# Optimization experiments

Measured on AMD Instinct MI355X. Metric: run time of the kernel, lower is better.

## Reference

```python
import jax, jax.numpy as jnp
import numpy as np

IN, OUT, RANK, ALPHA, GS = 4096, 4096, 16, 32, 64
SCALING = ALPHA / RANK  # alpha / rank = 2.0


def setup_inputs() -> dict:
    key = jax.random.key(0)
    k1, k2, k3, k4, k5 = jax.random.split(key, 5)
    x = jax.random.normal(k1, (4, 2048, IN), dtype=jnp.float32)
    # signed int4 codes in [-8, 7]
    q_w = jax.random.randint(k2, (OUT, IN), -8, 8, dtype=jnp.int32)
    # per-group absmax scales (positive, small)
    scales = jax.random.uniform(k3, (OUT, IN // GS), dtype=jnp.float32) * 0.02 + 1e-3
    lora_A = jax.random.normal(k4, (RANK, IN), dtype=jnp.float32) * 0.02
    lora_B = jax.random.normal(k5, (OUT, RANK), dtype=jnp.float32) * 0.02
    return {"x": x, "q_w": q_w, "scales": scales, "lora_A": lora_A, "lora_B": lora_B}


def reference(x, q_w, scales, lora_A, lora_B):
    # Dequantize 4-bit base weight: blockwise symmetric, group_size=GS along in_features.
    # W[o, g*GS + j] = q[o, g*GS + j] * scales[o, g]
    W = (q_w.astype(jnp.float32).reshape(OUT, IN // GS, GS)
         * scales[:, :, None]).reshape(OUT, IN)
    # Frozen base layer: y = x @ W^T (Linear4bit, no bias)
    base_output = jnp.einsum('bsi,oi->bso', x, W)
    # LoRA branch (dropout p=0 -> identity): B(A(x)) * (alpha/rank)
    lora_output = jnp.einsum('bsr,or->bso', jnp.einsum('bsi,ri->bsr', x, lora_A), lora_B) * SCALING
    return base_output + lora_output
```

## Files before the change

kernel.cpp:

```cpp
#include <hip/hip_runtime.h>
#include <hip/hip_bf16.h>


typedef unsigned short u16;
typedef __attribute__((ext_vector_type(8))) short bf16x8;
typedef __attribute__((ext_vector_type(4))) float f32x4;
typedef __attribute__((ext_vector_type(4))) int i32x4;

#define M_DIM 8192
#define N_DIM 4096
#define K_DIM 4096
#define BK 64
#define KT_MAIN 64
#define NT 65

__device__ static inline u16 f2bf(float f) {
    union { float f; unsigned u; } v; v.f = f;
    unsigned r = v.u + 0x7fffu + ((v.u >> 16) & 1u);
    return (u16)(r >> 16);
}

__device__ static inline void gload16(const void* g, void* s) {
    __builtin_amdgcn_global_load_lds(
        (const __attribute__((address_space(1))) void*)g,
        (__attribute__((address_space(3))) void*)s, 16, 0, 0);
}

__global__ __launch_bounds__(256) void prep_kernel(
        const int* __restrict__ q, const float* __restrict__ scales,
        const float* __restrict__ lora_B, const float* __restrict__ x,
        const float* __restrict__ lora_A,
        u16* __restrict__ Wb, u16* __restrict__ B2,
        u16* __restrict__ xb, u16* __restrict__ t2) {
    const int tid = threadIdx.x;
    int b = blockIdx.x;
    if (b < 1024) {
        const int w = tid >> 6, l = tid & 63;
        const int rb = b * 8 + w * 2;
        float acc[2][16];
#pragma unroll
        for (int j = 0; j < 2; ++j)
#pragma unroll
            for (int r = 0; r < 16; ++r) acc[j][r] = 0.f;

        for (int i = 0; i < 16; ++i) {
            int k0 = i * 256 + l * 4;
            f32x4 x0 = __builtin_nontemporal_load(
                            (const f32x4*)&x[(size_t)rb * K_DIM + k0]);
            f32x4 x1 = __builtin_nontemporal_load(
                            (const f32x4*)&x[(size_t)(rb + 1) * K_DIM + k0]);
            ushort4 o0, o1;
            o0.x = f2bf(x0.x); o0.y = f2bf(x0.y); o0.z = f2bf(x0.z); o0.w = f2bf(x0.w);
            o1.x = f2bf(x1.x); o1.y = f2bf(x1.y); o1.z = f2bf(x1.z); o1.w = f2bf(x1.w);
            *(ushort4*)&xb[(size_t)rb * K_DIM + k0]       = o0;
            *(ushort4*)&xb[(size_t)(rb + 1) * K_DIM + k0] = o1;
#pragma unroll
            for (int r = 0; r < 16; ++r) {
                f32x4 av = *(const f32x4*)&lora_A[(size_t)r * K_DIM + k0];
                acc[0][r] += x0.x * av.x + x0.y * av.y + x0.z * av.z + x0.w * av.w;
                acc[1][r] += x1.x * av.x + x1.y * av.y + x1.z * av.z + x1.w * av.w;
            }
        }
#pragma unroll
        for (int j = 0; j < 2; ++j)
#pragma unroll
            for (int r = 0; r < 16; ++r) {
                float v = acc[j][r];
                v += __shfl_xor(v, 32); v += __shfl_xor(v, 16);
                v += __shfl_xor(v, 8);  v += __shfl_xor(v, 4);
                v += __shfl_xor(v, 2);  v += __shfl_xor(v, 1);
                acc[j][r] = v;
            }
        float lo = 0.f, hi = 0.f;
#pragma unroll
        for (int j = 0; j < 2; ++j)
#pragma unroll
            for (int c = 0; c < 8; ++c)
                if (l == j * 32 + c) { lo = acc[j][2 * c]; hi = acc[j][2 * c + 1]; }
        unsigned pack = (unsigned)f2bf(2.0f * lo) | ((unsigned)f2bf(2.0f * hi) << 16);
        *(unsigned*)&t2[(size_t)(rb + (l >> 5)) * 64 + (l & 31) * 2] = pack;
    } else if (b < 9216) {
        int idx = (b - 1024) * 256 + tid;
        int o  = idx >> 9;
        int kc = (idx & 511) << 3;
        float s = scales[(o << 6) + (kc >> 6)];
        const i32x4* qp = (const i32x4*)(q + (size_t)o * K_DIM + kc);
        i32x4 q0 = __builtin_nontemporal_load(qp);
        i32x4 q1 = __builtin_nontemporal_load(qp + 1);
        ushort4 r0, r1;
        r0.x = f2bf((float)q0.x * s); r0.y = f2bf((float)q0.y * s);
        r0.z = f2bf((float)q0.z * s); r0.w = f2bf((float)q0.w * s);
        r1.x = f2bf((float)q1.x * s); r1.y = f2bf((float)q1.y * s);
        r1.z = f2bf((float)q1.z * s); r1.w = f2bf((float)q1.w * s);
        *(ushort4*)&Wb[(size_t)o * K_DIM + kc]     = r0;
        *(ushort4*)&Wb[(size_t)o * K_DIM + kc + 4] = r1;
    } else {
        int idx = (b - 9216) * 256 + tid;
        int o = idx >> 6, r = idx & 63;
        B2[idx] = (r < 16) ? f2bf(lora_B[o * 16 + r]) : (u16)0;
    }
}

__global__ __launch_bounds__(512, 2) void qlora_gemm(
        const u16* __restrict__ xb, const u16* __restrict__ Wb,
        const u16* __restrict__ t2, const u16* __restrict__ B2,
        float* __restrict__ out) {
    __shared__ u16 lds[2][32768];
    int bid = blockIdx.x;
    int x8 = bid & 7, sq = bid >> 3;
    int bm = (x8 & 1) * 16 + (sq & 15);
    int bn = (x8 >> 1) * 4 + (sq >> 4);
    const int tid = threadIdx.x, w = tid >> 6, l = tid & 63;
    const int wr = w >> 2, wc = w & 3;
    const int fr = l & 15, fq = l >> 4;
    const int s0 = fq ^ (fr & 7);

    const int sw16 = ((l & 7) ^ ((l >> 3) & 7)) << 4;
    const int rl   = w * 8 + (l >> 3);
    const int rA0  = bm * 256 + rl;
    const int rB0  = bn * 256 + rl;
    char* ldsC = (char*)&lds[0][0];
    const int dst = w * 1024 + l * 16;

    const int arow = (wr * 128 + fr) * 128;
    const int brow = 32768 + (wc * 64 + fr) * 128;

    f32x4 acc[8][4] = {};
    bf16x8 a0[8], b0[4], a1[8], b1[4];

    auto stage = [&](int kt, int buf) {
        char* base = ldsC + buf * 65536;
        if (kt < KT_MAIN) {
            size_t ko = (size_t)kt * 128;
#pragma unroll
            for (int o = 0; o < 4; ++o) {
                gload16((const char*)xb + ((size_t)(rA0 + o * 64) * 8192 + sw16) + ko,
                        base + dst + o * 8192);
                gload16((const char*)Wb + ((size_t)(rB0 + o * 64) * 8192 + sw16) + ko,
                        base + 32768 + dst + o * 8192);
            }
        } else {
#pragma unroll
            for (int o = 0; o < 4; ++o) {
                gload16((const char*)t2 + ((size_t)(rA0 + o * 64) * 128 + sw16),
                        base + dst + o * 8192);
                gload16((const char*)B2 + ((size_t)(rB0 + o * 64) * 128 + sw16),
                        base + 32768 + dst + o * 8192);
            }
        }
    };

    auto read0 = [&](const char* cb) {
#pragma unroll
        for (int j = 0; j < 4; ++j)
            b0[j] = *(const bf16x8*)(cb + brow + j * 2048 + s0 * 16);
#pragma unroll
        for (int i = 0; i < 8; ++i)
            a0[i] = *(const bf16x8*)(cb + arow + i * 2048 + s0 * 16);
    };
    auto read1 = [&](const char* cb) {
#pragma unroll
        for (int j = 0; j < 4; ++j)
            b1[j] = *(const bf16x8*)(cb + brow + j * 2048 + (s0 ^ 4) * 16);
#pragma unroll
        for (int i = 0; i < 8; ++i)
            a1[i] = *(const bf16x8*)(cb + arow + i * 2048 + (s0 ^ 4) * 16);
    };
    auto mfma0 = [&]() {
        __builtin_amdgcn_s_setprio(1);
#pragma unroll
        for (int i = 0; i < 8; ++i)
#pragma unroll
            for (int j = 0; j < 4; ++j)
                acc[i][j] = __builtin_amdgcn_mfma_f32_16x16x32_bf16(
                                a0[i], b0[j], acc[i][j], 0, 0, 0);
        __builtin_amdgcn_s_setprio(0);
    };
    auto mfma1 = [&]() {
        __builtin_amdgcn_s_setprio(1);
#pragma unroll
        for (int i = 0; i < 8; ++i)
#pragma unroll
            for (int j = 0; j < 4; ++j)
                acc[i][j] = __builtin_amdgcn_mfma_f32_16x16x32_bf16(
                                a1[i], b1[j], acc[i][j], 0, 0, 0);
        __builtin_amdgcn_s_setprio(0);
    };

    stage(0, 0);
    stage(1, 1);
    asm volatile("s_waitcnt vmcnt(8)" ::: "memory");
    __builtin_amdgcn_s_barrier();
    asm volatile("" ::: "memory");

    read0(ldsC);
    asm volatile("s_waitcnt lgkmcnt(0)" ::: "memory");
    __builtin_amdgcn_sched_barrier(0);
    read1(ldsC);
    __builtin_amdgcn_sched_barrier(0);
    mfma0();
    __builtin_amdgcn_sched_barrier(0);
    asm volatile("s_waitcnt lgkmcnt(0)" ::: "memory");
    asm volatile("s_waitcnt vmcnt(0)" ::: "memory");
    __builtin_amdgcn_s_barrier();
    asm volatile("" ::: "memory");

    for (int t = 1; t < NT; ++t) {
        const char* cb = ldsC + (t & 1) * 65536;
        if (t + 1 < NT) stage(t + 1, (t + 1) & 1);
        read0(cb);
        __builtin_amdgcn_sched_barrier(0);
        mfma1();
        __builtin_amdgcn_sched_barrier(0);
        asm volatile("s_waitcnt lgkmcnt(0)" ::: "memory");
        read1(cb);
        __builtin_amdgcn_sched_barrier(0);
        mfma0();
        __builtin_amdgcn_sched_barrier(0);
        asm volatile("s_waitcnt lgkmcnt(0)" ::: "memory");
        asm volatile("s_waitcnt vmcnt(0)" ::: "memory");
        __builtin_amdgcn_s_barrier();
        asm volatile("" ::: "memory");
    }
    mfma1();

    float* obase = out + (size_t)(bm * 256 + wr * 128 + fq * 4) * N_DIM
                       + bn * 256 + wc * 64 + fr;
#pragma unroll
    for (int i = 0; i < 8; ++i)
#pragma unroll
        for (int j = 0; j < 4; ++j)
#pragma unroll
            for (int r = 0; r < 4; ++r)
                obase[(size_t)(i * 16 + r) * N_DIM + j * 16] = acc[i][j][r];
}

extern "C" void kernel_launch(void* const* d_in, const int* in_sizes, int n_in,
                              void* d_out, int out_size, void* d_ws, size_t ws_size,
                              hipStream_t stream) {
    const float* x      = (const float*)d_in[0];
    const int*   qw     = (const int*)d_in[1];
    const float* scales = (const float*)d_in[2];
    const float* lora_A = (const float*)d_in[3];
    const float* lora_B = (const float*)d_in[4];
    float* out = (float*)d_out;

    char* ws = (char*)d_ws;
    u16* xb = (u16*)(ws);
    u16* Wb = (u16*)(ws + 67108864);
    u16* t2 = (u16*)(ws + 100663296);
    u16* B2 = (u16*)(ws + 101711872);

    prep_kernel<<<10240, 256, 0, stream>>>(qw, scales, lora_B, x, lora_A,
                                           Wb, B2, xb, t2);
    qlora_gemm<<<dim3(512), 512, 0, stream>>>(xb, Wb, t2, B2, out);
}
```

Baseline: 320.8 us.

## Use triple-buffered BK=32 LDS pipeline and shrink LoRA pad to K=32

The GEMM K-tile drops from 64 to 32, and the two LDS buffers of 64KB become three of 32KB. Loads are now issued two stages ahead, with a partial vmcnt wait so global loads overlap compute, and the LDS swizzle is reworked for the 64-byte rows. The LoRA intermediate and B matrices are padded to 32 instead of 64, so the extra LoRA tile is half as large. The prep kernel now processes four rows per warp. The cost is twice as many barriers and iterations per tile, plus lower LDS use per block, which may let more blocks fit on a CU.

```diff
diff --git a/kernel.cpp b/kernel.cpp
--- a/kernel.cpp
+++ b/kernel.cpp
@@ -10,9 +10,8 @@
 #define M_DIM 8192
 #define N_DIM 4096
 #define K_DIM 4096
-#define BK 64
-#define KT_MAIN 64
-#define NT 65
+#define KT_MAIN 128
+#define NT 129
 
 __device__ static inline u16 f2bf(float f) {
     union { float f; unsigned u; } v; v.f = f;
@@ -34,35 +33,38 @@
         u16* __restrict__ xb, u16* __restrict__ t2) {
     const int tid = threadIdx.x;
     int b = blockIdx.x;
-    if (b < 1024) {
+    if (b < 512) {
         const int w = tid >> 6, l = tid & 63;
-        const int rb = b * 8 + w * 2;
-        float acc[2][16];
-#pragma unroll
-        for (int j = 0; j < 2; ++j)
+        const int rb = b * 16 + w * 4;
+        float acc[4][16];
+#pragma unroll
+        for (int j = 0; j < 4; ++j)
 #pragma unroll
             for (int r = 0; r < 16; ++r) acc[j][r] = 0.f;
 
         for (int i = 0; i < 16; ++i) {
             int k0 = i * 256 + l * 4;
-            f32x4 x0 = __builtin_nontemporal_load(
-                            (const f32x4*)&x[(size_t)rb * K_DIM + k0]);
-            f32x4 x1 = __builtin_nontemporal_load(
-                            (const f32x4*)&x[(size_t)(rb + 1) * K_DIM + k0]);
-            ushort4 o0, o1;
-            o0.x = f2bf(x0.x); o0.y = f2bf(x0.y); o0.z = f2bf(x0.z); o0.w = f2bf(x0.w);
-            o1.x = f2bf(x1.x); o1.y = f2bf(x1.y); o1.z = f2bf(x1.z); o1.w = f2bf(x1.w);
-            *(ushort4*)&xb[(size_t)rb * K_DIM + k0]       = o0;
-            *(ushort4*)&xb[(size_t)(rb + 1) * K_DIM + k0] = o1;
+            f32x4 xv[4];
+#pragma unroll
+            for (int j = 0; j < 4; ++j) {
+                xv[j] = __builtin_nontemporal_load(
+                            (const f32x4*)&x[(size_t)(rb + j) * K_DIM + k0]);
+                ushort4 o4;
+                o4.x = f2bf(xv[j].x); o4.y = f2bf(xv[j].y);
+                o4.z = f2bf(xv[j].z); o4.w = f2bf(xv[j].w);
+                *(ushort4*)&xb[(size_t)(rb + j) * K_DIM + k0] = o4;
+            }
 #pragma unroll
             for (int r = 0; r < 16; ++r) {
                 f32x4 av = *(const f32x4*)&lora_A[(size_t)r * K_DIM + k0];
-                acc[0][r] += x0.x * av.x + x0.y * av.y + x0.z * av.z + x0.w * av.w;
-                acc[1][r] += x1.x * av.x + x1.y * av.y + x1.z * av.z + x1.w * av.w;
+#pragma unroll
+                for (int j = 0; j < 4; ++j)
+                    acc[j][r] += xv[j].x * av.x + xv[j].y * av.y
+                               + xv[j].z * av.z + xv[j].w * av.w;
             }
         }
 #pragma unroll
-        for (int j = 0; j < 2; ++j)
+        for (int j = 0; j < 4; ++j)
 #pragma unroll
             for (int r = 0; r < 16; ++r) {
                 float v = acc[j][r];
@@ -71,16 +73,16 @@
                 v += __shfl_xor(v, 2);  v += __shfl_xor(v, 1);
                 acc[j][r] = v;
             }
-        float lo = 0.f, hi = 0.f;
-#pragma unroll
-        for (int j = 0; j < 2; ++j)
-#pragma unroll
-            for (int c = 0; c < 8; ++c)
-                if (l == j * 32 + c) { lo = acc[j][2 * c]; hi = acc[j][2 * c + 1]; }
-        unsigned pack = (unsigned)f2bf(2.0f * lo) | ((unsigned)f2bf(2.0f * hi) << 16);
-        *(unsigned*)&t2[(size_t)(rb + (l >> 5)) * 64 + (l & 31) * 2] = pack;
-    } else if (b < 9216) {
-        int idx = (b - 1024) * 256 + tid;
+        float v = 0.f;
+#pragma unroll
+        for (int j = 0; j < 4; ++j)
+#pragma unroll
+            for (int r = 0; r < 16; ++r)
+                if (l == j * 16 + r) v = acc[j][r];
+        t2[(size_t)(rb + (l >> 4)) * 32 + (l & 15)]      = f2bf(2.0f * v);
+        t2[(size_t)(rb + (l >> 4)) * 32 + 16 + (l & 15)] = 0;
+    } else if (b < 8704) {
+        int idx = (b - 512) * 256 + tid;
         int o  = idx >> 9;
         int kc = (idx & 511) << 3;
         float s = scales[(o << 6) + (kc >> 6)];
@@ -95,8 +97,8 @@
         *(ushort4*)&Wb[(size_t)o * K_DIM + kc]     = r0;
         *(ushort4*)&Wb[(size_t)o * K_DIM + kc + 4] = r1;
     } else {
-        int idx = (b - 9216) * 256 + tid;
-        int o = idx >> 6, r = idx & 63;
+        int idx = (b - 8704) * 256 + tid;
+        int o = idx >> 5, r = idx & 31;
         B2[idx] = (r < 16) ? f2bf(lora_B[o * 16 + r]) : (u16)0;
     }
 }
@@ -105,7 +107,7 @@
         const u16* __restrict__ xb, const u16* __restrict__ Wb,
         const u16* __restrict__ t2, const u16* __restrict__ B2,
         float* __restrict__ out) {
-    __shared__ u16 lds[2][32768];
+    __shared__ u16 lds[3][16384];
     int bid = blockIdx.x;
     int x8 = bid & 7, sq = bid >> 3;
     int bm = (x8 & 1) * 16 + (sq & 15);
@@ -113,116 +115,113 @@
     const int tid = threadIdx.x, w = tid >> 6, l = tid & 63;
     const int wr = w >> 2, wc = w & 3;
     const int fr = l & 15, fq = l >> 4;
-    const int s0 = fq ^ (fr & 7);
-
-    const int sw16 = ((l & 7) ^ ((l >> 3) & 7)) << 4;
-    const int rl   = w * 8 + (l >> 3);
-    const int rA0  = bm * 256 + rl;
-    const int rB0  = bn * 256 + rl;
+    const int phys = fq ^ ((fr >> 2) & 3);
+
+    const int rS   = tid >> 2;
+    const int swz  = ((tid & 3) ^ ((tid >> 4) & 3)) << 4;
     char* ldsC = (char*)&lds[0][0];
-    const int dst = w * 1024 + l * 16;
-
-    const int arow = (wr * 128 + fr) * 128;
-    const int brow = 32768 + (wc * 64 + fr) * 128;
+    const int dstA = tid * 16;
+    const int dstB = 16384 + tid * 16;
+
+    const int arow = (wr * 128 + fr) * 64 + (phys << 4);
+    const int brow = 16384 + (wc * 64 + fr) * 64 + (phys << 4);
 
     f32x4 acc[8][4] = {};
-    bf16x8 a0[8], b0[4], a1[8], b1[4];
-
-    auto stage = [&](int kt, int buf) {
-        char* base = ldsC + buf * 65536;
+    bf16x8 aA[8], bA[4], aB[8], bB[4];
+
+    auto stage = [&](int kt) {
+        char* base = ldsC + (kt % 3) * 32768;
         if (kt < KT_MAIN) {
-            size_t ko = (size_t)kt * 128;
-#pragma unroll
-            for (int o = 0; o < 4; ++o) {
-                gload16((const char*)xb + ((size_t)(rA0 + o * 64) * 8192 + sw16) + ko,
-                        base + dst + o * 8192);
-                gload16((const char*)Wb + ((size_t)(rB0 + o * 64) * 8192 + sw16) + ko,
-                        base + 32768 + dst + o * 8192);
-            }
+            size_t ko = (size_t)kt * 64;
+            gload16((const char*)xb + ((size_t)(bm * 256 + rS)       * 8192 + swz) + ko, base + dstA);
+            gload16((const char*)xb + ((size_t)(bm * 256 + rS + 128) * 8192 + swz) + ko, base + dstA + 8192);
+            gload16((const char*)Wb + ((size_t)(bn * 256 + rS)       * 8192 + swz) + ko, base + dstB);
+            gload16((const char*)Wb + ((size_t)(bn * 256 + rS + 128) * 8192 + swz) + ko, base + dstB + 8192);
         } else {
-#pragma unroll
-            for (int o = 0; o < 4; ++o) {
-                gload16((const char*)t2 + ((size_t)(rA0 + o * 64) * 128 + sw16),
-                        base + dst + o * 8192);
-                gload16((const char*)B2 + ((size_t)(rB0 + o * 64) * 128 + sw16),
-                        base + 32768 + dst + o * 8192);
-            }
+            gload16((const char*)t2 + ((size_t)(bm * 256 + rS)       * 64 + swz), base + dstA);
+            gload16((const char*)t2 + ((size_t)(bm * 256 + rS + 128) * 64 + swz), base + dstA + 8192);
+            gload16((const char*)B2 + ((size_t)(bn * 256 + rS)       * 64 + swz), base + dstB);
+            gload16((const char*)B2 + ((size_t)(bn * 256 + rS + 128) * 64 + swz), base + dstB + 8192);
         }
     };
 
-    auto read0 = [&](const char* cb) {
-#pragma unroll
-        for (int j = 0; j < 4; ++j)
-            b0[j] = *(const bf16x8*)(cb + brow + j * 2048 + s0 * 16);
-#pragma unroll
-        for (int i = 0; i < 8; ++i)
-            a0[i] = *(const bf16x8*)(cb + arow + i * 2048 + s0 * 16);
-    };
-    auto read1 = [&](const char* cb) {
-#pragma unroll
-        for (int j = 0; j < 4; ++j)
-            b1[j] = *(const bf16x8*)(cb + brow + j * 2048 + (s0 ^ 4) * 16);
-#pragma unroll
-        for (int i = 0; i < 8; ++i)
-            a1[i] = *(const bf16x8*)(cb + arow + i * 2048 + (s0 ^ 4) * 16);
-    };
-    auto mfma0 = [&]() {
+    auto readA = [&](const char* cb) {
+#pragma unroll
+        for (int j = 0; j < 4; ++j)
+            bA[j] = *(const bf16x8*)(cb + brow + j * 1024);
+#pragma unroll
+        for (int i = 0; i < 8; ++i)
+            aA[i] = *(const bf16x8*)(cb + arow + i * 1024);
+    };
+    auto readB = [&](const char* cb) {
+#pragma unroll
+        for (int j = 0; j < 4; ++j)
+            bB[j] = *(const bf16x8*)(cb + brow + j * 1024);
+#pragma unroll
+        for (int i = 0; i < 8; ++i)
+            aB[i] = *(const bf16x8*)(cb + arow + i * 1024);
+    };
+    auto mfmaA = [&]() {
         __builtin_amdgcn_s_setprio(1);
 #pragma unroll
         for (int i = 0; i < 8; ++i)
 #pragma unroll
             for (int j = 0; j < 4; ++j)
                 acc[i][j] = __builtin_amdgcn_mfma_f32_16x16x32_bf16(
-                                a0[i], b0[j], acc[i][j], 0, 0, 0);
+                                aA[i], bA[j], acc[i][j], 0, 0, 0);
         __builtin_amdgcn_s_setprio(0);
     };
-    auto mfma1 = [&]() {
+    auto mfmaB = [&]() {
         __builtin_amdgcn_s_setprio(1);
 #pragma unroll
         for (int i = 0; i < 8; ++i)
 #pragma unroll
             for (int j = 0; j < 4; ++j)
                 acc[i][j] = __builtin_amdgcn_mfma_f32_16x16x32_bf16(
-                                a1[i], b1[j], acc[i][j], 0, 0, 0);
+                                aB[i], bB[j], acc[i][j], 0, 0, 0);
         __builtin_amdgcn_s_setprio(0);
     };
 
-    stage(0, 0);
-    stage(1, 1);
-    asm volatile("s_waitcnt vmcnt(8)" ::: "memory");
+    stage(0);
+    stage(1);
+    asm volatile("s_waitcnt vmcnt(4)" ::: "memory");
     __builtin_amdgcn_s_barrier();
     asm volatile("" ::: "memory");
-
-    read0(ldsC);
+    readA(ldsC);
+    __builtin_amdgcn_sched_barrier(0);
+
+    for (int it = 0; it < 64; ++it) {
+        int T = 2 * it;
+        stage(T + 2);
+        __builtin_amdgcn_sched_barrier(0);
+        asm volatile("s_waitcnt lgkmcnt(0)" ::: "memory");
+        __builtin_amdgcn_sched_barrier(0);
+        mfmaA();
+        __builtin_amdgcn_sched_barrier(0);
+        asm volatile("s_waitcnt vmcnt(4)" ::: "memory");
+        __builtin_amdgcn_s_barrier();
+        asm volatile("" ::: "memory");
+        readB(ldsC + ((T + 1) % 3) * 32768);
+        __builtin_amdgcn_sched_barrier(0);
+
+        if (it < 63) stage(T + 3);
+        __builtin_amdgcn_sched_barrier(0);
+        asm volatile("s_waitcnt lgkmcnt(0)" ::: "memory");
+        __builtin_amdgcn_sched_barrier(0);
+        mfmaB();
+        __builtin_amdgcn_sched_barrier(0);
+        if (it < 63)
+            asm volatile("s_waitcnt vmcnt(4)" ::: "memory");
+        else
+            asm volatile("s_waitcnt vmcnt(0)" ::: "memory");
+        __builtin_amdgcn_s_barrier();
+        asm volatile("" ::: "memory");
+        readA(ldsC + ((T + 2) % 3) * 32768);
+        __builtin_amdgcn_sched_barrier(0);
+    }
     asm volatile("s_waitcnt lgkmcnt(0)" ::: "memory");
     __builtin_amdgcn_sched_barrier(0);
-    read1(ldsC);
-    __builtin_amdgcn_sched_barrier(0);
-    mfma0();
-    __builtin_amdgcn_sched_barrier(0);
-    asm volatile("s_waitcnt lgkmcnt(0)" ::: "memory");
-    asm volatile("s_waitcnt vmcnt(0)" ::: "memory");
-    __builtin_amdgcn_s_barrier();
-    asm volatile("" ::: "memory");
-
-    for (int t = 1; t < NT; ++t) {
-        const char* cb = ldsC + (t & 1) * 65536;
-        if (t + 1 < NT) stage(t + 1, (t + 1) & 1);
-        read0(cb);
-        __builtin_amdgcn_sched_barrier(0);
-        mfma1();
-        __builtin_amdgcn_sched_barrier(0);
-        asm volatile("s_waitcnt lgkmcnt(0)" ::: "memory");
-        read1(cb);
-        __builtin_amdgcn_sched_barrier(0);
-        mfma0();
-        __builtin_amdgcn_sched_barrier(0);
-        asm volatile("s_waitcnt lgkmcnt(0)" ::: "memory");
-        asm volatile("s_waitcnt vmcnt(0)" ::: "memory");
-        __builtin_amdgcn_s_barrier();
-        asm volatile("" ::: "memory");
-    }
-    mfma1();
+    mfmaA();
 
     float* obase = out + (size_t)(bm * 256 + wr * 128 + fq * 4) * N_DIM
                        + bn * 256 + wc * 64 + fr;
@@ -249,9 +248,9 @@
     u16* xb = (u16*)(ws);
     u16* Wb = (u16*)(ws + 67108864);
     u16* t2 = (u16*)(ws + 100663296);
-    u16* B2 = (u16*)(ws + 101711872);
-
-    prep_kernel<<<10240, 256, 0, stream>>>(qw, scales, lora_B, x, lora_A,
-                                           Wb, B2, xb, t2);
+    u16* B2 = (u16*)(ws + 101187584);
+
+    prep_kernel<<<9216, 256, 0, stream>>>(qw, scales, lora_B, x, lora_A,
+                                          Wb, B2, xb, t2);
     qlora_gemm<<<dim3(512), 512, 0, stream>>>(xb, Wb, t2, B2, out);
 }
```

Measured after the change: 346.0 us. 7.8% more time.

## Restructure GEMM main loop software pipeline and widen LoRA-A prep rows per warp

Applied to the files above, without the earlier changes.

The GEMM main loop is reordered so each iteration reads the second half-tile, issues the next global stage, runs the first MFMA batch, syncs, then prefetches the next tile's first half from LDS before running the second MFMA batch. The prologue now stages only one tile instead of two. Separately, the prep kernel processes four rows per warp instead of two, so each lora_A load is reused across more rows and half as many blocks are launched. It also writes the zero padding of t2 explicitly. The pipeline change alters how LDS reads overlap with MFMA work, and the wider prep rows raise register use.

```diff
diff --git a/kernel.cpp b/kernel.cpp
--- a/kernel.cpp
+++ b/kernel.cpp
@@ -34,35 +34,38 @@
         u16* __restrict__ xb, u16* __restrict__ t2) {
     const int tid = threadIdx.x;
     int b = blockIdx.x;
-    if (b < 1024) {
+    if (b < 512) {
         const int w = tid >> 6, l = tid & 63;
-        const int rb = b * 8 + w * 2;
-        float acc[2][16];
-#pragma unroll
-        for (int j = 0; j < 2; ++j)
+        const int rb = b * 16 + w * 4;
+        float acc[4][16];
+#pragma unroll
+        for (int j = 0; j < 4; ++j)
 #pragma unroll
             for (int r = 0; r < 16; ++r) acc[j][r] = 0.f;
 
         for (int i = 0; i < 16; ++i) {
             int k0 = i * 256 + l * 4;
-            f32x4 x0 = __builtin_nontemporal_load(
-                            (const f32x4*)&x[(size_t)rb * K_DIM + k0]);
-            f32x4 x1 = __builtin_nontemporal_load(
-                            (const f32x4*)&x[(size_t)(rb + 1) * K_DIM + k0]);
-            ushort4 o0, o1;
-            o0.x = f2bf(x0.x); o0.y = f2bf(x0.y); o0.z = f2bf(x0.z); o0.w = f2bf(x0.w);
-            o1.x = f2bf(x1.x); o1.y = f2bf(x1.y); o1.z = f2bf(x1.z); o1.w = f2bf(x1.w);
-            *(ushort4*)&xb[(size_t)rb * K_DIM + k0]       = o0;
-            *(ushort4*)&xb[(size_t)(rb + 1) * K_DIM + k0] = o1;
+            f32x4 xv[4];
+#pragma unroll
+            for (int j = 0; j < 4; ++j) {
+                xv[j] = __builtin_nontemporal_load(
+                            (const f32x4*)&x[(size_t)(rb + j) * K_DIM + k0]);
+                ushort4 o4;
+                o4.x = f2bf(xv[j].x); o4.y = f2bf(xv[j].y);
+                o4.z = f2bf(xv[j].z); o4.w = f2bf(xv[j].w);
+                *(ushort4*)&xb[(size_t)(rb + j) * K_DIM + k0] = o4;
+            }
 #pragma unroll
             for (int r = 0; r < 16; ++r) {
                 f32x4 av = *(const f32x4*)&lora_A[(size_t)r * K_DIM + k0];
-                acc[0][r] += x0.x * av.x + x0.y * av.y + x0.z * av.z + x0.w * av.w;
-                acc[1][r] += x1.x * av.x + x1.y * av.y + x1.z * av.z + x1.w * av.w;
+#pragma unroll
+                for (int j = 0; j < 4; ++j)
+                    acc[j][r] += xv[j].x * av.x + xv[j].y * av.y
+                               + xv[j].z * av.z + xv[j].w * av.w;
             }
         }
 #pragma unroll
-        for (int j = 0; j < 2; ++j)
+        for (int j = 0; j < 4; ++j)
 #pragma unroll
             for (int r = 0; r < 16; ++r) {
                 float v = acc[j][r];
@@ -71,16 +74,19 @@
                 v += __shfl_xor(v, 2);  v += __shfl_xor(v, 1);
                 acc[j][r] = v;
             }
-        float lo = 0.f, hi = 0.f;
-#pragma unroll
-        for (int j = 0; j < 2; ++j)
-#pragma unroll
-            for (int c = 0; c < 8; ++c)
-                if (l == j * 32 + c) { lo = acc[j][2 * c]; hi = acc[j][2 * c + 1]; }
-        unsigned pack = (unsigned)f2bf(2.0f * lo) | ((unsigned)f2bf(2.0f * hi) << 16);
-        *(unsigned*)&t2[(size_t)(rb + (l >> 5)) * 64 + (l & 31) * 2] = pack;
-    } else if (b < 9216) {
-        int idx = (b - 1024) * 256 + tid;
+        float v = 0.f;
+#pragma unroll
+        for (int j = 0; j < 4; ++j)
+#pragma unroll
+            for (int r = 0; r < 16; ++r)
+                if (l == j * 16 + r) v = acc[j][r];
+        int row = rb + (l >> 4), col = l & 15;
+        t2[(size_t)row * 64 + col]      = f2bf(2.0f * v);
+        t2[(size_t)row * 64 + 16 + col] = 0;
+        t2[(size_t)row * 64 + 32 + col] = 0;
+        t2[(size_t)row * 64 + 48 + col] = 0;
+    } else if (b < 8704) {
+        int idx = (b - 512) * 256 + tid;
         int o  = idx >> 9;
         int kc = (idx & 511) << 3;
         float s = scales[(o << 6) + (kc >> 6)];
@@ -95,7 +101,7 @@
         *(ushort4*)&Wb[(size_t)o * K_DIM + kc]     = r0;
         *(ushort4*)&Wb[(size_t)o * K_DIM + kc + 4] = r1;
     } else {
-        int idx = (b - 9216) * 256 + tid;
+        int idx = (b - 8704) * 256 + tid;
         int o = idx >> 6, r = idx & 63;
         B2[idx] = (r < 16) ? f2bf(lora_B[o * 16 + r]) : (u16)0;
     }
@@ -188,41 +194,41 @@
     };
 
     stage(0, 0);
-    stage(1, 1);
-    asm volatile("s_waitcnt vmcnt(8)" ::: "memory");
-    __builtin_amdgcn_s_barrier();
-    asm volatile("" ::: "memory");
-
-    read0(ldsC);
-    asm volatile("s_waitcnt lgkmcnt(0)" ::: "memory");
-    __builtin_amdgcn_sched_barrier(0);
-    read1(ldsC);
-    __builtin_amdgcn_sched_barrier(0);
-    mfma0();
-    __builtin_amdgcn_sched_barrier(0);
-    asm volatile("s_waitcnt lgkmcnt(0)" ::: "memory");
     asm volatile("s_waitcnt vmcnt(0)" ::: "memory");
     __builtin_amdgcn_s_barrier();
     asm volatile("" ::: "memory");
 
-    for (int t = 1; t < NT; ++t) {
+#pragma unroll
+    for (int j = 0; j < 4; ++j)
+        b0[j] = *(const bf16x8*)(ldsC + brow + j * 2048 + s0 * 16);
+#pragma unroll
+    for (int i = 0; i < 8; ++i)
+        a0[i] = *(const bf16x8*)(ldsC + arow + i * 2048 + s0 * 16);
+
+    for (int t = 0; t < NT; ++t) {
         const char* cb = ldsC + (t & 1) * 65536;
+
+        read1(cb);
         if (t + 1 < NT) stage(t + 1, (t + 1) & 1);
-        read0(cb);
-        __builtin_amdgcn_sched_barrier(0);
-        mfma1();
-        __builtin_amdgcn_sched_barrier(0);
-        asm volatile("s_waitcnt lgkmcnt(0)" ::: "memory");
-        read1(cb);
-        __builtin_amdgcn_sched_barrier(0);
+        __builtin_amdgcn_sched_barrier(0);
+
         mfma0();
         __builtin_amdgcn_sched_barrier(0);
+
         asm volatile("s_waitcnt lgkmcnt(0)" ::: "memory");
         asm volatile("s_waitcnt vmcnt(0)" ::: "memory");
         __builtin_amdgcn_s_barrier();
         asm volatile("" ::: "memory");
+
+        if (t + 1 < NT) {
+            const char* nb = ldsC + ((t + 1) & 1) * 65536;
+            read0(nb);
+        }
+        __builtin_amdgcn_sched_barrier(0);
+
+        mfma1();
+        __builtin_amdgcn_sched_barrier(0);
     }
-    mfma1();
 
     float* obase = out + (size_t)(bm * 256 + wr * 128 + fq * 4) * N_DIM
                        + bn * 256 + wc * 64 + fr;
@@ -251,7 +257,7 @@
     u16* t2 = (u16*)(ws + 100663296);
     u16* B2 = (u16*)(ws + 101711872);
 
-    prep_kernel<<<10240, 256, 0, stream>>>(qw, scales, lora_B, x, lora_A,
-                                           Wb, B2, xb, t2);
+    prep_kernel<<<9728, 256, 0, stream>>>(qw, scales, lora_B, x, lora_A,
+                                          Wb, B2, xb, t2);
     qlora_gemm<<<dim3(512), 512, 0, stream>>>(xb, Wb, t2, B2, out);
 }
```

Measured after the change: 327.5 us. 2.1% more time.
